# Kernel optimization log

Hardware: AMD Instinct MI355X
Metric: run time of the kernel (lower is better)

The kernel has to match this reference:

```python
import jax, jax.numpy as jnp
import numpy as np

S = 8192        # seq_length
H2 = 1024       # 2 * lstm_hidden_size
A = 2048        # attention_hidden_size
E = 768         # embedding_dim == pos_embedding_dim


def _bahdanau_weights(sentence, length, ctx, W_s, b_s, W_c, b_c, v, b_v):
    # sentence: [1, S, H2], ctx: [1, E_ctx]
    u = jnp.einsum('bsh,ha->bsa', sentence, W_s) + b_s \
        + (ctx @ W_c + b_c)[:, None, :]                    # [1, S, A]
    e = jnp.einsum('bsa,a->bs', jnp.tanh(u), v) + b_v       # [1, S]
    mask = jnp.arange(S)[None, :] >= length[:, None]        # [1, S] key mask
    e = jnp.where(mask, -jnp.inf, e)
    all_inf = jnp.all(mask, axis=1)                         # [1]
    # guard fully-masked rows so softmax stays finite, then zero them (matches torch)
    e_safe = jnp.where(all_inf[:, None], jnp.zeros_like(e), e)
    w = jax.nn.softmax(e_safe, axis=1)
    return jnp.where(all_inf[:, None], 0.0, w)              # [1, S]


def setup_inputs() -> dict:
    key = jax.random.key(0)
    ks = jax.random.split(key, 24)
    f = jax.random.normal
    sc_s = 1.0 / np.sqrt(H2)
    sc_c = 1.0 / np.sqrt(E)
    sc_v = 1.0 / np.sqrt(A)
    inp = {
        'sentence': f(ks[0], (1, S, H2), jnp.float32),
        'length': jax.random.randint(ks[1], (1,), 0, S),
        'pos_embedding': f(ks[2], (1, E), jnp.float32),
        'cardinal_phrase_embedding': f(ks[3], (1, E), jnp.float32),
        'headline_embedding': f(ks[4], (1, E), jnp.float32),
    }
    i = 5
    for tag in ('p', 'c', 'h'):
        inp[f'W_sent_{tag}'] = f(ks[i], (H2, A), jnp.float32) * sc_s; i += 1
        inp[f'b_sent_{tag}'] = f(ks[i], (A,), jnp.float32) * sc_s; i += 1
        inp[f'W_ctx_{tag}'] = f(ks[i], (E, A), jnp.float32) * sc_c; i += 1
        inp[f'b_ctx_{tag}'] = f(ks[i], (A,), jnp.float32) * sc_c; i += 1
        inp[f'v_{tag}'] = f(ks[i], (A,), jnp.float32) * sc_v; i += 1
        inp[f'bv_{tag}'] = f(ks[i], (), jnp.float32) * sc_v; i += 1
    return inp


def reference(sentence, length, pos_embedding, cardinal_phrase_embedding,
              headline_embedding,
              W_sent_p, b_sent_p, W_ctx_p, b_ctx_p, v_p, bv_p,
              W_sent_c, b_sent_c, W_ctx_c, b_ctx_c, v_c, bv_c,
              W_sent_h, b_sent_h, W_ctx_h, b_ctx_h, v_h, bv_h):
    w_pos = _bahdanau_weights(sentence, length, pos_embedding,
                              W_sent_p, b_sent_p, W_ctx_p, b_ctx_p, v_p, bv_p)
    w_card = _bahdanau_weights(sentence, length, cardinal_phrase_embedding,
                               W_sent_c, b_sent_c, W_ctx_c, b_ctx_c, v_c, bv_c)
    w_head = _bahdanau_weights(sentence, length, headline_embedding,
                               W_sent_h, b_sent_h, W_ctx_h, b_ctx_h, v_h, bv_h)
    fused = (w_pos + w_card + w_head) / 3.0                 # [1, S]
    return jnp.einsum('bs,bsh->bh', fused, sentence)        # [1, H2]
```

## Files before the change

### kernel.cpp

```cpp
#include <hip/hip_runtime.h>
#include <hip/hip_bf16.h>
#include <stdint.h>


namespace {

constexpr int S = 8192;
constexpr int H = 1024;
constexpr int A = 2048;
constexpr int E = 768;

typedef __bf16 bf16x8 __attribute__((ext_vector_type(8)));
typedef float f32x4 __attribute__((ext_vector_type(4)));

__device__ __forceinline__ void gl_lds16(const void* g, void* l) {
  __builtin_amdgcn_global_load_lds(
      (const __attribute__((address_space(1))) void*)g,
      (__attribute__((address_space(3))) void*)l, 16, 0, 0);
}

__global__ __launch_bounds__(256)
void k_prep(const float* __restrict__ sentence, __bf16* __restrict__ sentB,
            const float* __restrict__ Wp, const float* __restrict__ Wc_s,
            const float* __restrict__ Wh, __bf16* __restrict__ WtB,
            const float* __restrict__ ctx_p, const float* __restrict__ ctx_c,
            const float* __restrict__ ctx_h,
            const float* __restrict__ Wcx_p, const float* __restrict__ Wcx_c,
            const float* __restrict__ Wcx_h,
            const float* __restrict__ bs_p, const float* __restrict__ bs_c,
            const float* __restrict__ bs_h,
            const float* __restrict__ bc_p, const float* __restrict__ bc_c,
            const float* __restrict__ bc_h,
            float* __restrict__ ctxb,
            const int* __restrict__ length, float* __restrict__ out, int n_out) {
  __shared__ float tile[64][65];
  int b = blockIdx.x;
  int t = threadIdx.x;

  if (b < 4096) {
    int len = min(max(length[0], 0), S);
    int lenp = (len + 127) & ~127;
    if (b * 2 >= lenp) return;
    int g = b * 256 + t;
    const float4* s4 = (const float4*)sentence + (size_t)g * 2;
    float4 a = s4[0], c = s4[1];
    bf16x8 o;
    o[0] = (__bf16)a.x; o[1] = (__bf16)a.y; o[2] = (__bf16)a.z; o[3] = (__bf16)a.w;
    o[4] = (__bf16)c.x; o[5] = (__bf16)c.y; o[6] = (__bf16)c.z; o[7] = (__bf16)c.w;
    *((bf16x8*)sentB + g) = o;
  } else if (b < 5632) {
    int r = b - 4096;
    int head = r >> 9; r &= 511;
    const float* W = head == 0 ? Wp : (head == 1 ? Wc_s : Wh);
    __bf16* dst = WtB + (size_t)head * A * H;
    int a0 = (r & 31) * 64;
    int k0 = (r >> 5) * 64;
#pragma unroll
    for (int i = 0; i < 16; ++i) {
      int idx = t + i * 256;
      int rr = idx >> 6, cc = idx & 63;
      tile[cc][rr] = W[(size_t)(k0 + rr) * A + a0 + cc];
    }
    __syncthreads();
#pragma unroll
    for (int i = 0; i < 16; ++i) {
      int idx = t + i * 256;
      int al = idx >> 6, kl = idx & 63;
      dst[(size_t)(a0 + al) * H + k0 + kl] = (__bf16)tile[al][kl];
    }
  } else if (b < 6208) {
    int r = b - 5632;
    int head = r / 192; r %= 192;
    int ablk = r & 7;
    int echk = r >> 3;
    const float* ctx = head == 0 ? ctx_p : (head == 1 ? ctx_c : ctx_h);
    const float* Wc  = head == 0 ? Wcx_p : (head == 1 ? Wcx_c : Wcx_h);
    int a = ablk * 256 + t;
    float s = 0.f;
    int e0 = echk * 32;
#pragma unroll 8
    for (int e = e0; e < e0 + 32; ++e) s = fmaf(ctx[e], Wc[(size_t)e * A + a], s);
    if (echk == 0) {
      const float* bs = head == 0 ? bs_p : (head == 1 ? bs_c : bs_h);
      const float* bc = head == 0 ? bc_p : (head == 1 ? bc_c : bc_h);
      s += bs[a] + bc[a];
    }
    atomicAdd(&ctxb[head * A + a], s);
  } else {
    float4 z = {0.f, 0.f, 0.f, 0.f};
    for (int i = t; i * 4 < n_out; i += 256) ((float4*)out)[i] = z;
  }
}

__global__ __launch_bounds__(256)
void k_gemm_e(const __bf16* __restrict__ sentB, const __bf16* __restrict__ WtB,
              const float* __restrict__ ctxb,
              const float* __restrict__ v_p, const float* __restrict__ v_c,
              const float* __restrict__ v_h,
              const int* __restrict__ length, float* __restrict__ e_out) {
  int m0 = blockIdx.x * 128;
  int len = min(max(length[0], 0), S);
  if (m0 >= len) return;
  int n0 = blockIdx.y * 128;
  int head = blockIdx.z;
  const float* v  = head == 0 ? v_p : (head == 1 ? v_c : v_h);
  const __bf16* Wt = WtB + (size_t)head * A * H;
  const float* cb = ctxb + head * A;
  float* e_h = e_out + head * S;

  __shared__ __align__(16) __bf16 lsA[3 * 4096];
  __shared__ __align__(16) __bf16 lsB[3 * 4096];
  __shared__ float e_part[128];

  int tid = threadIdx.x;
  if (tid < 128) e_part[tid] = 0.f;

  int lane = tid & 63;
  int wave = tid >> 6;
  int wm = wave >> 1, wn = wave & 1;
  int quad = lane >> 4, l16 = lane & 15;

  f32x4 acc[4][4];
#pragma unroll
  for (int i = 0; i < 4; ++i)
#pragma unroll
    for (int j = 0; j < 4; ++j) acc[i][j] = (f32x4){0.f, 0.f, 0.f, 0.f};

  const __bf16* gA0 = sentB + (size_t)(m0 + (tid >> 2)) * H + ((tid & 3) * 8);
  const __bf16* gA1 = gA0 + (size_t)64 * H;
  const __bf16* gB0 = Wt + (size_t)(n0 + (tid >> 2)) * H + ((tid & 3) * 8);
  const __bf16* gB1 = gB0 + (size_t)64 * H;

#define STAGE(bufi, kk)                                           \
  do {                                                            \
    gl_lds16(gA0 + (kk), lsA + (bufi) * 4096 + tid * 8);          \
    gl_lds16(gA1 + (kk), lsA + (bufi) * 4096 + 2048 + tid * 8);   \
    gl_lds16(gB0 + (kk), lsB + (bufi) * 4096 + tid * 8);          \
    gl_lds16(gB1 + (kk), lsB + (bufi) * 4096 + 2048 + tid * 8);   \
  } while (0)

#define COMPUTE(bufi)                                                                     \
  do {                                                                                    \
    bf16x8 af[4], bfv[4];                                                                 \
    _Pragma("unroll")                                                                     \
    for (int i = 0; i < 4; ++i) {                                                         \
      af[i]  = *(const bf16x8*)&lsA[(bufi) * 4096 + (wm * 64 + i * 16 + l16) * 32 + quad * 8]; \
      bfv[i] = *(const bf16x8*)&lsB[(bufi) * 4096 + (wn * 64 + i * 16 + l16) * 32 + quad * 8]; \
    }                                                                                     \
    _Pragma("unroll")                                                                     \
    for (int i = 0; i < 4; ++i)                                                           \
      _Pragma("unroll")                                                                   \
      for (int j = 0; j < 4; ++j)                                                         \
        acc[i][j] = __builtin_amdgcn_mfma_f32_16x16x32_bf16(af[i], bfv[j], acc[i][j], 0, 0, 0); \
  } while (0)

  STAGE(0, 0);
  STAGE(1, 32);
  int cur = 0, nxt = 2;
#pragma unroll 1
  for (int t = 0; t < 31; ++t) {
    asm volatile("s_waitcnt vmcnt(4)\n\ts_barrier" ::: "memory");
    if (t < 30) STAGE(nxt, (t + 2) * 32);
    COMPUTE(cur);
    cur = cur == 2 ? 0 : cur + 1;
    nxt = nxt == 2 ? 0 : nxt + 1;
  }
  asm volatile("s_waitcnt vmcnt(0)\n\ts_barrier" ::: "memory");
  COMPUTE(cur);

#undef STAGE
#undef COMPUTE

  float vj[4], cbj[4];
#pragma unroll
  for (int j = 0; j < 4; ++j) {
    int col = n0 + wn * 64 + j * 16 + l16;
    vj[j] = v[col];
    cbj[j] = cb[col];
  }
#pragma unroll
  for (int i = 0; i < 4; ++i) {
#pragma unroll
    for (int r = 0; r < 4; ++r) {
      float p = 0.f;
#pragma unroll
      for (int j = 0; j < 4; ++j) {
        float u = acc[i][j][r] + cbj[j];
        float ex = __expf(2.f * u);
        float th = 1.f - 2.f / (ex + 1.f);
        p = fmaf(th, vj[j], p);
      }
      p += __shfl_xor(p, 1);
      p += __shfl_xor(p, 2);
      p += __shfl_xor(p, 4);
      p += __shfl_xor(p, 8);
      if (l16 == 0) atomicAdd(&e_part[wm * 64 + i * 16 + quad * 4 + r], p);
    }
  }
  __syncthreads();
  if (tid < 128) atomicAdd(&e_h[m0 + tid], e_part[tid]);
}

__global__ void k_out(const float* __restrict__ sent, const float* __restrict__ e_arr,
                      const int* __restrict__ length, float* __restrict__ out) {
  int len = min(max(length[0], 0), S);
  int r0 = blockIdx.x * 16;
  if (r0 >= len) return;
  int tid = threadIdx.x;

  __shared__ float red[3][4];
  __shared__ float sstat[6];
  __shared__ float wrow[16];

#pragma unroll
  for (int h = 0; h < 3; ++h) {
    const float* e_h = e_arr + h * S;
    float m = -3.4e38f;
    for (int s = tid; s < len; s += 256) m = fmaxf(m, e_h[s]);
#pragma unroll
    for (int o = 32; o >= 1; o >>= 1) m = fmaxf(m, __shfl_xor(m, o));
    if ((tid & 63) == 0) red[h][tid >> 6] = m;
  }
  __syncthreads();
  if (tid < 3) sstat[tid * 2] = fmaxf(fmaxf(red[tid][0], red[tid][1]),
                                      fmaxf(red[tid][2], red[tid][3]));
  __syncthreads();
#pragma unroll
  for (int h = 0; h < 3; ++h) {
    const float* e_h = e_arr + h * S;
    float mm = sstat[h * 2];
    float ss = 0.f;
    for (int s = tid; s < len; s += 256) ss += __expf(e_h[s] - mm);
#pragma unroll
    for (int o = 32; o >= 1; o >>= 1) ss += __shfl_xor(ss, o);
    if ((tid & 63) == 0) red[h][tid >> 6] = ss;
  }
  __syncthreads();
  if (tid < 3) sstat[tid * 2 + 1] = red[tid][0] + red[tid][1] + red[tid][2] + red[tid][3];
  __syncthreads();

  if (tid < 16 && r0 + tid < len) {
    int r = r0 + tid;
    wrow[tid] = (__expf(e_arr[r] - sstat[0]) / sstat[1] +
                 __expf(e_arr[S + r] - sstat[2]) / sstat[3] +
                 __expf(e_arr[2 * S + r] - sstat[4]) / sstat[5]) * (1.f / 3.f);
  }
  __syncthreads();

  int col = tid * 4;
  int rend = min(r0 + 16, len);
  float4 acc = {0.f, 0.f, 0.f, 0.f};
  for (int r = r0; r < rend; ++r) {
    float w = wrow[r - r0];
    float4 x = *(const float4*)(sent + (size_t)r * H + col);
    acc.x = fmaf(w, x.x, acc.x);
    acc.y = fmaf(w, x.y, acc.y);
    acc.z = fmaf(w, x.z, acc.z);
    acc.w = fmaf(w, x.w, acc.w);
  }
  atomicAdd(&out[col + 0], acc.x);
  atomicAdd(&out[col + 1], acc.y);
  atomicAdd(&out[col + 2], acc.z);
  atomicAdd(&out[col + 3], acc.w);
}

}

extern "C" void kernel_launch(void* const* d_in, const int* in_sizes, int n_in,
                              void* d_out, int out_size, void* d_ws, size_t ws_size,
                              hipStream_t stream) {
  const float* sentence = (const float*)d_in[0];
  const int* length     = (const int*)d_in[1];
  const float* ctx_p = (const float*)d_in[2];
  const float* ctx_c = (const float*)d_in[3];
  const float* ctx_h = (const float*)d_in[4];
  const float* W_s[3] = {(const float*)d_in[5],  (const float*)d_in[11], (const float*)d_in[17]};
  const float* b_s[3] = {(const float*)d_in[6],  (const float*)d_in[12], (const float*)d_in[18]};
  const float* W_c[3] = {(const float*)d_in[7],  (const float*)d_in[13], (const float*)d_in[19]};
  const float* b_c[3] = {(const float*)d_in[8],  (const float*)d_in[14], (const float*)d_in[20]};
  const float* v_[3]  = {(const float*)d_in[9],  (const float*)d_in[15], (const float*)d_in[21]};
  float* out = (float*)d_out;

  char* ws = (char*)d_ws;
  __bf16* sentB = (__bf16*)(ws);
  __bf16* WtB   = (__bf16*)(ws + 16777216);
  float* ctxb   = (float*)(ws + 29360128);
  float* e_arr  = (float*)(ws + 29384704);

  hipMemsetAsync(ctxb, 0, (A * 3 + S * 3) * sizeof(float), stream);

  k_prep<<<6209, 256, 0, stream>>>(sentence, sentB,
                                   W_s[0], W_s[1], W_s[2], WtB,
                                   ctx_p, ctx_c, ctx_h,
                                   W_c[0], W_c[1], W_c[2],
                                   b_s[0], b_s[1], b_s[2],
                                   b_c[0], b_c[1], b_c[2], ctxb,
                                   length, out, out_size);
  k_gemm_e<<<dim3(S / 128, A / 128, 3), 256, 0, stream>>>(sentB, WtB, ctxb,
                                                          v_[0], v_[1], v_[2], length, e_arr);
  k_out<<<S / 16, 256, 0, stream>>>(sentence, e_arr, length, out);
}
```

Before: 234.3 us.

## Swizzle GEMM LDS layout, drop memset and atomics in context projection

The GEMM tiles are now stored in LDS with an XOR swizzle on the 16-byte column chunk, keyed on the row, to cut bank conflicts on the MFMA fragment reads. The barrier is now issued as a builtin followed by a sched_barrier. In the prep kernel the context projection now gives each thread the full 768-length reduction and a plain store, replacing the split-E atomicAdd scheme. The separate hipMemsetAsync is removed, and the zeroing of e_arr and out moves into prep blocks. The trade-off is that only 24 blocks now do the long serial context dot products, so that stage has less parallelism.

```diff
diff --git a/kernel.cpp b/kernel.cpp
--- a/kernel.cpp
+++ b/kernel.cpp
@@ -31,7 +31,7 @@
             const float* __restrict__ bs_h,
             const float* __restrict__ bc_p, const float* __restrict__ bc_c,
             const float* __restrict__ bc_h,
-            float* __restrict__ ctxb,
+            float* __restrict__ ctxb, float* __restrict__ e_arr,
             const int* __restrict__ length, float* __restrict__ out, int n_out) {
   __shared__ float tile[64][65];
   int b = blockIdx.x;
@@ -68,27 +68,27 @@
       int al = idx >> 6, kl = idx & 63;
       dst[(size_t)(a0 + al) * H + k0 + kl] = (__bf16)tile[al][kl];
     }
-  } else if (b < 6208) {
+  } else if (b < 5656) {
     int r = b - 5632;
-    int head = r / 192; r %= 192;
+    int head = r >> 3;
     int ablk = r & 7;
-    int echk = r >> 3;
     const float* ctx = head == 0 ? ctx_p : (head == 1 ? ctx_c : ctx_h);
     const float* Wc  = head == 0 ? Wcx_p : (head == 1 ? Wcx_c : Wcx_h);
+    const float* bs  = head == 0 ? bs_p : (head == 1 ? bs_c : bs_h);
+    const float* bc  = head == 0 ? bc_p : (head == 1 ? bc_c : bc_h);
     int a = ablk * 256 + t;
-    float s = 0.f;
-    int e0 = echk * 32;
+    float s = bs[a] + bc[a];
 #pragma unroll 8
-    for (int e = e0; e < e0 + 32; ++e) s = fmaf(ctx[e], Wc[(size_t)e * A + a], s);
-    if (echk == 0) {
-      const float* bs = head == 0 ? bs_p : (head == 1 ? bs_c : bs_h);
-      const float* bc = head == 0 ? bc_p : (head == 1 ? bc_c : bc_h);
-      s += bs[a] + bc[a];
+    for (int e = 0; e < E; ++e) s = fmaf(ctx[e], Wc[(size_t)e * A + a], s);
+    ctxb[head * A + a] = s;
+  } else {
+    int idx = (b - 5656) * 256 + t;
+    float4 z = {0.f, 0.f, 0.f, 0.f};
+    int total = 6144 + (n_out >> 2);
+    for (int i = idx; i < total; i += 2048) {
+      if (i < 6144) ((float4*)e_arr)[i] = z;
+      else ((float4*)out)[i - 6144] = z;
     }
-    atomicAdd(&ctxb[head * A + a], s);
-  } else {
-    float4 z = {0.f, 0.f, 0.f, 0.f};
-    for (int i = t; i * 4 < n_out; i += 256) ((float4*)out)[i] = z;
   }
 }
 
@@ -119,6 +119,7 @@
   int wave = tid >> 6;
   int wm = wave >> 1, wn = wave & 1;
   int quad = lane >> 4, l16 = lane & 15;
+  int sw = (quad ^ (l16 & 3)) << 3;
 
   f32x4 acc[4][4];
 #pragma unroll
@@ -126,9 +127,11 @@
 #pragma unroll
     for (int j = 0; j < 4; ++j) acc[i][j] = (f32x4){0.f, 0.f, 0.f, 0.f};
 
-  const __bf16* gA0 = sentB + (size_t)(m0 + (tid >> 2)) * H + ((tid & 3) * 8);
+  int srow = tid >> 2;
+  int scol = ((tid & 3) ^ (srow & 3)) * 8;
+  const __bf16* gA0 = sentB + (size_t)(m0 + srow) * H + scol;
   const __bf16* gA1 = gA0 + (size_t)64 * H;
-  const __bf16* gB0 = Wt + (size_t)(n0 + (tid >> 2)) * H + ((tid & 3) * 8);
+  const __bf16* gB0 = Wt + (size_t)(n0 + srow) * H + scol;
   const __bf16* gB1 = gB0 + (size_t)64 * H;
 
 #define STAGE(bufi, kk)                                           \
@@ -139,33 +142,38 @@
     gl_lds16(gB1 + (kk), lsB + (bufi) * 4096 + 2048 + tid * 8);   \
   } while (0)
 
-#define COMPUTE(bufi)                                                                     \
-  do {                                                                                    \
-    bf16x8 af[4], bfv[4];                                                                 \
-    _Pragma("unroll")                                                                     \
-    for (int i = 0; i < 4; ++i) {                                                         \
-      af[i]  = *(const bf16x8*)&lsA[(bufi) * 4096 + (wm * 64 + i * 16 + l16) * 32 + quad * 8]; \
-      bfv[i] = *(const bf16x8*)&lsB[(bufi) * 4096 + (wn * 64 + i * 16 + l16) * 32 + quad * 8]; \
-    }                                                                                     \
-    _Pragma("unroll")                                                                     \
-    for (int i = 0; i < 4; ++i)                                                           \
-      _Pragma("unroll")                                                                   \
-      for (int j = 0; j < 4; ++j)                                                         \
+#define COMPUTE(bufi)                                                                           \
+  do {                                                                                          \
+    bf16x8 af[4], bfv[4];                                                                       \
+    _Pragma("unroll")                                                                           \
+    for (int i = 0; i < 4; ++i)                                                                 \
+      af[i] = *(const bf16x8*)&lsA[(bufi) * 4096 + (wm * 64 + i * 16 + l16) * 32 + sw];         \
+    _Pragma("unroll")                                                                           \
+    for (int j = 0; j < 4; ++j)                                                                 \
+      bfv[j] = *(const bf16x8*)&lsB[(bufi) * 4096 + (wn * 64 + j * 16 + l16) * 32 + sw];        \
+    _Pragma("unroll")                                                                           \
+    for (int i = 0; i < 4; ++i)                                                                 \
+      _Pragma("unroll")                                                                         \
+      for (int j = 0; j < 4; ++j)                                                               \
         acc[i][j] = __builtin_amdgcn_mfma_f32_16x16x32_bf16(af[i], bfv[j], acc[i][j], 0, 0, 0); \
   } while (0)
 
   STAGE(0, 0);
   STAGE(1, 32);
-  int cur = 0, nxt = 2;
+  int cur = 0, pf = 2;
 #pragma unroll 1
   for (int t = 0; t < 31; ++t) {
-    asm volatile("s_waitcnt vmcnt(4)\n\ts_barrier" ::: "memory");
-    if (t < 30) STAGE(nxt, (t + 2) * 32);
+    asm volatile("s_waitcnt vmcnt(4)");
+    __builtin_amdgcn_s_barrier();
+    __builtin_amdgcn_sched_barrier(0);
+    if (t < 30) STAGE(pf, (t + 2) * 32);
     COMPUTE(cur);
     cur = cur == 2 ? 0 : cur + 1;
-    nxt = nxt == 2 ? 0 : nxt + 1;
-  }
-  asm volatile("s_waitcnt vmcnt(0)\n\ts_barrier" ::: "memory");
+    pf = pf == 2 ? 0 : pf + 1;
+  }
+  asm volatile("s_waitcnt vmcnt(0)");
+  __builtin_amdgcn_s_barrier();
+  __builtin_amdgcn_sched_barrier(0);
   COMPUTE(cur);
 
 #undef STAGE
@@ -287,14 +295,12 @@
   float* ctxb   = (float*)(ws + 29360128);
   float* e_arr  = (float*)(ws + 29384704);
 
-  hipMemsetAsync(ctxb, 0, (A * 3 + S * 3) * sizeof(float), stream);
-
-  k_prep<<<6209, 256, 0, stream>>>(sentence, sentB,
+  k_prep<<<5664, 256, 0, stream>>>(sentence, sentB,
                                    W_s[0], W_s[1], W_s[2], WtB,
                                    ctx_p, ctx_c, ctx_h,
                                    W_c[0], W_c[1], W_c[2],
                                    b_s[0], b_s[1], b_s[2],
-                                   b_c[0], b_c[1], b_c[2], ctxb,
+                                   b_c[0], b_c[1], b_c[2], ctxb, e_arr,
                                    length, out, out_size);
   k_gemm_e<<<dim3(S / 128, A / 128, 3), 256, 0, stream>>>(sentB, WtB, ctxb,
                                                           v_[0], v_[1], v_[2], length, e_arr);
```

New measurement: 279.1 us. +19.1%, slower.
